# Kernel tuning notes

Hardware: AMD Instinct MI355X
Metric: run time of the kernel (lower is better)

## Reference

```python
import jax, jax.numpy as jnp
import numpy as np

R = 128          # input voxel grid resolution
N = 200000
C_IN = 128
C_OUT = 256
G = 32           # group-norm groups
EPS = 1e-5


def _build_sparse_structure():
    """Generate random sparse voxel coords, downsample map, and 3x3x3 neighbor table."""
    rng = np.random.default_rng(0)
    lin = rng.choice(R ** 3, size=N, replace=False)
    cx, cy, cz = lin // (R * R), (lin // R) % R, lin % R
    # downsample by 2: coords // 2 on a (R//2)^3 grid
    Rd = R // 2
    key = ((cx // 2) * Rd + (cy // 2)) * Rd + (cz // 2)
    uk, inv = np.unique(key, return_inverse=True)   # uk sorted
    M = len(uk)
    dx, dy, dz = uk // (Rd * Rd), (uk // Rd) % Rd, uk % Rd
    # 27-neighbor table for submanifold 3x3x3 conv on the downsampled coords
    nbr = np.full((M, 27), -1, np.int32)
    k = 0
    for ox in (-1, 0, 1):
        for oy in (-1, 0, 1):
            for oz in (-1, 0, 1):
                nx, ny, nz = dx + ox, dy + oy, dz + oz
                valid = (nx >= 0) & (nx < Rd) & (ny >= 0) & (ny < Rd) & (nz >= 0) & (nz < Rd)
                nkey = (nx * Rd + ny) * Rd + nz
                pos = np.clip(np.searchsorted(uk, nkey), 0, M - 1)
                found = valid & (uk[pos] == nkey)
                nbr[:, k] = np.where(found, pos, -1).astype(np.int32)
                k += 1
    return inv.astype(np.int32), nbr, M


def setup_inputs() -> dict:
    pool_seg, nbr_idx, M = _build_sparse_structure()
    key = jax.random.key(0)
    ks = jax.random.split(key, 12)
    f32 = jnp.float32
    feats = jax.random.normal(ks[0], (N, C_IN), f32)
    s1 = float(1.0 / np.sqrt(27 * C_IN))
    s2 = float(1.0 / np.sqrt(27 * C_OUT))
    return {
        "feats": feats,
        "gn1_w": 1.0 + 0.1 * jax.random.normal(ks[1], (C_IN,), f32),
        "gn1_b": 0.1 * jax.random.normal(ks[2], (C_IN,), f32),
        "W1": jax.random.normal(ks[3], (27, C_IN, C_OUT), f32) * s1,
        "b1": 0.01 * jax.random.normal(ks[4], (C_OUT,), f32),
        "gn2_w": 1.0 + 0.1 * jax.random.normal(ks[5], (C_OUT,), f32),
        "gn2_b": 0.1 * jax.random.normal(ks[6], (C_OUT,), f32),
        "W2": jax.random.normal(ks[7], (27, C_OUT, C_OUT), f32) * s2,
        "b2": 0.01 * jax.random.normal(ks[8], (C_OUT,), f32),
        "Wskip": jax.random.normal(ks[9], (C_IN, C_OUT), f32) * float(1.0 / np.sqrt(C_IN)),
        "bskip": 0.01 * jax.random.normal(ks[10], (C_OUT,), f32),
        "pool_seg": jnp.asarray(pool_seg),
        "nbr_idx": jnp.asarray(nbr_idx),
        "num_down": int(M),
    }


def _group_norm(x, gamma, beta):
    # batch size 1: normalize each group over all voxels and its channels
    n, c = x.shape
    xg = x.reshape(n, G, c // G)
    mu = xg.mean(axis=(0, 2), keepdims=True)
    var = xg.var(axis=(0, 2), keepdims=True)
    xn = (xg - mu) * jax.lax.rsqrt(var + EPS)
    return xn.reshape(n, c) * gamma + beta


def _sparse_conv3(x, W, b, nbr_idx):
    # submanifold 3x3x3 conv: out[i] = sum_k W[k] @ x[nbr[i,k]] (missing nbr -> 0)
    idx = jnp.maximum(nbr_idx, 0)
    mask = (nbr_idx >= 0).astype(x.dtype)
    acc = jnp.zeros((x.shape[0], W.shape[2]), x.dtype)
    for k in range(27):
        acc = acc + (x[idx[:, k]] * mask[:, k:k + 1]) @ W[k]
    return acc + b


def reference(feats, gn1_w, gn1_b, W1, b1, gn2_w, gn2_b, W2, b2, Wskip, bskip,
              pool_seg, nbr_idx, num_down):
    # act_layers: GroupNorm32 + SiLU on the full-resolution sparse tensor
    h = jax.nn.silu(_group_norm(feats, gn1_w, gn1_b))
    # SparseDownsample(2): average features of voxels sharing a coord//2 cell
    cnt = jax.ops.segment_sum(jnp.ones((feats.shape[0], 1), feats.dtype),
                              pool_seg, num_segments=num_down)
    inv_cnt = 1.0 / jnp.maximum(cnt, 1.0)
    h_d = jax.ops.segment_sum(h, pool_seg, num_segments=num_down) * inv_cnt
    x_d = jax.ops.segment_sum(feats, pool_seg, num_segments=num_down) * inv_cnt
    # out_layers: conv3 -> GN -> SiLU -> conv3
    h1 = _sparse_conv3(h_d, W1, b1, nbr_idx)
    h2 = jax.nn.silu(_group_norm(h1, gn2_w, gn2_b))
    h3 = _sparse_conv3(h2, W2, b2, nbr_idx)
    # skip: 1x1 sparse conv on downsampled input, then add (same coord set)
    skip = x_d @ Wskip + bskip
    return h3 + skip
```

## Files before the change

### kernel.cpp

```cpp
#include <hip/hip_runtime.h>
#include <hip/hip_bf16.h>
#include <stdint.h>

typedef __hip_bfloat16 bf16;
typedef __attribute__((ext_vector_type(8))) __bf16 bf16x8;
typedef __attribute__((ext_vector_type(4))) float f32x4;

#define GN_EPS 1e-5f

__device__ __forceinline__ float silu_f(float x) {
  return x / (1.f + __expf(-x));
}

__device__ __forceinline__ float ldf(const void* p, size_t i, int f) {
  return f ? ((const float*)p)[i]
           : __bfloat162float(((const bf16*)p)[i]);
}

__device__ __forceinline__ void llds16(const void* g, void* l) {
  __builtin_amdgcn_global_load_lds(
      (const __attribute__((address_space(1))) unsigned int*)g,
      (__attribute__((address_space(3))) unsigned int*)l, 16, 0, 0);
}

__device__ __forceinline__ void gload16(bf16x8& d, const bf16* addr) {
  asm volatile("global_load_dwordx4 %0, %1, off"
               : "=&v"(d) : "v"(addr) : "memory");
}

__global__ void detect_k(const void* __restrict__ gn1w, int* __restrict__ flag) {
  if (threadIdx.x == 0 && blockIdx.x == 0) {
    const unsigned short* u = (const unsigned short*)gn1w;
    float mx = 0.f;
    for (int i = 0; i < 128; ++i) {
      unsigned int b = ((unsigned int)u[i]) << 16;
      float v = __uint_as_float(b);
      v = fabsf(v);
      if (!isnan(v) && v > mx) mx = v;
    }
    flag[0] = (mx > 1e4f) ? 1 : 0;
  }
}

__global__ void transpose_k(const void* __restrict__ in, bf16* __restrict__ out,
                            int CI, int CO, const int* __restrict__ flagp) {
  const int f = *flagp;
  int k = blockIdx.y;
  int ntco = CO >> 5;
  int tci = blockIdx.x / ntco, tco = blockIdx.x % ntco;
  __shared__ float t[32][33];
  int tx = threadIdx.x & 31, ty = threadIdx.x >> 5;
  size_t base = (size_t)k * CI * CO;
  bf16* dst = out + base;
#pragma unroll
  for (int j = 0; j < 4; ++j)
    t[ty + 8 * j][tx] =
        ldf(in, base + (size_t)(tci * 32 + ty + 8 * j) * CO + tco * 32 + tx, f);
  __syncthreads();
#pragma unroll
  for (int j = 0; j < 4; ++j)
    dst[(size_t)tci * (CO * 32) + (size_t)(tco * 32 + ty + 8 * j) * 32 + tx] =
        __float2bfloat16(t[tx][ty + 8 * j]);
}

__global__ void gn_stats_k(const void* __restrict__ x, float* __restrict__ raw,
                           int rows, int C, const int* __restrict__ flagp) {
  const int f = *flagp;
  int tid = threadIdx.x;
  int rpb = 256 / C;
  int c = tid & (C - 1);
  int stripe = tid / C;
  float s = 0.f, sq = 0.f;
  for (int r = blockIdx.x * rpb + stripe; r < rows; r += gridDim.x * rpb) {
    float v = ldf(x, (size_t)r * C + c, f);
    s += v; sq += v * v;
  }
  __shared__ float ls[256], lq[256];
  ls[tid] = s; lq[tid] = sq;
  __syncthreads();
  if (tid < 32) {
    int per = C >> 5;
    float as = 0.f, aq = 0.f;
    for (int st = 0; st < rpb; ++st)
      for (int e = 0; e < per; ++e) {
        int idx = st * C + tid * per + e;
        as += ls[idx]; aq += lq[idx];
      }
    atomicAdd(&raw[tid], as);
    atomicAdd(&raw[32 + tid], aq);
  }
}

__global__ void gn_fin_k(const float* __restrict__ raw, float* __restrict__ fin,
                         float count) {
  int g = threadIdx.x;
  if (g < 32) {
    float mu = raw[g] / count;
    float var = fmaxf(raw[32 + g] / count - mu * mu, 0.f);
    fin[g] = mu;
    fin[32 + g] = rsqrtf(var + GN_EPS);
  }
}

__global__ void slots_k(const int* __restrict__ seg, int* __restrict__ cnt,
                        int* __restrict__ slots, int N) {
  int i = blockIdx.x * 256 + threadIdx.x;
  if (i >= N) return;
  int s = seg[i];
  int p = atomicAdd(&cnt[s], 1);
  if (p < 8) slots[s * 8 + p] = i;
}

__global__ void down_k(const void* __restrict__ feats, const int* __restrict__ slots,
                       const int* __restrict__ cnt, const float* __restrict__ fin1,
                       const void* __restrict__ gw, const void* __restrict__ gb,
                       bf16* __restrict__ xd, bf16* __restrict__ hd, int M,
                       const int* __restrict__ flagp) {
  const int f = *flagp;
  int cell = blockIdx.x * 2 + (threadIdx.x >> 7);
  int c = threadIdx.x & 127;
  if (cell >= M) return;
  int n = min(cnt[cell], 8);
  int g = c >> 2;
  float mu = fin1[g], is = fin1[32 + g];
  float w = ldf(gw, c, f), b = ldf(gb, c, f);
  float xs = 0.f, hs = 0.f;
  for (int j = 0; j < n; ++j) {
    int v = slots[cell * 8 + j];
    float fv = ldf(feats, (size_t)v * 128 + c, f);
    xs += fv;
    hs += silu_f((fv - mu) * is * w + b);
  }
  float inv = 1.f / (float)max(n, 1);
  xd[(size_t)cell * 128 + c] = __float2bfloat16(xs * inv);
  hd[(size_t)cell * 128 + c] = __float2bfloat16(hs * inv);
}

__global__ void act2_k(bf16* __restrict__ h, const float* __restrict__ fin2,
                       const void* __restrict__ gw, const void* __restrict__ gb,
                       size_t total8, const int* __restrict__ flagp) {
  const int f = *flagp;
  size_t i = (size_t)blockIdx.x * 256 + threadIdx.x;
  if (i >= total8) return;
  int c0 = (int)((i * 8) & 255);
  int g = c0 >> 3;
  float mu = fin2[g], is = fin2[32 + g];
  bf16x8 v = *reinterpret_cast<bf16x8*>(h + i * 8);
  bf16x8 o;
#pragma unroll
  for (int j = 0; j < 8; ++j) {
    float x = (float)v[j];
    float t = (x - mu) * is * ldf(gw, c0 + j, f) + ldf(gb, c0 + j, f);
    o[j] = (__bf16)silu_f(t);
  }
  *reinterpret_cast<bf16x8*>(h + i * 8) = o;
}

template <int CIN, bool SKIP>
__global__ __launch_bounds__(512, 2) void conv_k(
    const bf16* __restrict__ A, const bf16* __restrict__ Wt,
    const void* __restrict__ bias, const void* __restrict__ bias2,
    const bf16* __restrict__ Xd, const int* __restrict__ nbr,
    void* __restrict__ out, int M, int nwg, const void* __restrict__ zp,
    const int* __restrict__ biasflagp, const int* __restrict__ outflagp) {
  constexpr int NCB = CIN / 32;
  constexpr int LOG_NCB = (CIN == 256) ? 3 : 2;
  constexpr int NT = 27 * NCB + (SKIP ? 4 : 0);
  __shared__ alignas(16) char smem[24576 + 10368];
  char* Aring = smem;
  int* nbrT = (int*)(smem + 24576);

  const int bflag = *biasflagp, oflag = *outflagp;
  const int tid = threadIdx.x;
  const int wave = tid >> 6, lane = tid & 63;
  const bool wlo = (wave < 6);

  int bid = blockIdx.x;
  int q = nwg >> 3, r8 = nwg & 7, xcd = bid & 7, ix = bid >> 3;
  int wg = (xcd < r8 ? xcd * (q + 1) : r8 * (q + 1) + (xcd - r8) * q) + ix;
  const int row0 = wg * 96;

  for (int i = tid; i < 27 * 96; i += 512) {
    int k = i / 96, r = i - k * 96;
    int g = row0 + r;
    int v = -1;
    if (g < M) v = nbr[(size_t)g * 27 + k];
    nbrT[i] = v;
  }
  __syncthreads();

  const int srow = lane >> 2;
  const int schk = lane & 3;

  auto stageA = [&](int t) {
    if (!wlo) return;
    char* Asl = Aring + (size_t)(t & 3) * 6144;
    const bool isW = (!SKIP) || (t < 27 * NCB);
    const int kk = t >> LOG_NCB;
    const int cb = isW ? (t & (NCB - 1)) : (t - 27 * NCB);
    const int cink = isW ? CIN : 128;
    const bf16* Ab = isW ? A : Xd;
    const int koff = cb * 32;
    int r = wave * 16 + srow;
    int src;
    if (isW) src = nbrT[kk * 96 + r];
    else { int g = row0 + r; src = (g < M) ? g : -1; }
    int lc = schk ^ ((r >> 1) & 3);
    const bf16* ga = (src >= 0) ? Ab + (size_t)src * cink + koff + lc * 8
                                : (const bf16*)zp;
    llds16(ga, Asl + (size_t)wave * 1024);
  };

  const int mrow = lane & 15, quad = lane >> 4;
  const int wr = wave >> 2, wc = wave & 3;
  const int cswz = (quad ^ ((mrow >> 1) & 3)) * 16;

  int beoff[4];
#pragma unroll
  for (int j = 0; j < 4; ++j)
    beoff[j] = (wc * 64 + j * 16 + mrow) * 32 + quad * 8;

  auto loadB = [&](bf16x8 (&dst)[4], int t) {
    const bool isW = (!SKIP) || (t < 27 * NCB);
    const int kk = t >> LOG_NCB;
    const int cb = isW ? (t & (NCB - 1)) : (t - 27 * NCB);
    const bf16* base = Wt +
        (isW ? (size_t)kk * (256 * CIN) : (size_t)27 * (256 * CIN)) +
        (size_t)cb * (256 * 32);
#pragma unroll
    for (int j = 0; j < 4; ++j) gload16(dst[j], base + beoff[j]);
  };

  f32x4 acc[3][4] = {};

  auto compute = [&](int t, const bf16x8 (&bv)[4]) {
    const char* As = Aring + (size_t)(t & 3) * 6144 +
                     (size_t)(wr * 48 + mrow) * 64 + cswz;
    bf16x8 af[3];
#pragma unroll
    for (int i = 0; i < 3; ++i)
      af[i] = *reinterpret_cast<const bf16x8*>(As + i * (16 * 64));
    __builtin_amdgcn_s_setprio(1);
#pragma unroll
    for (int i = 0; i < 3; ++i)
#pragma unroll
      for (int j = 0; j < 4; ++j)
        acc[i][j] = __builtin_amdgcn_mfma_f32_16x16x32_bf16(af[i], bv[j],
                                                            acc[i][j], 0, 0, 0);
    __builtin_amdgcn_s_setprio(0);
  };

#define VMW(a, b)                                                        \
  do {                                                                   \
    if (wlo) asm volatile("s_waitcnt vmcnt(" #a ")" ::: "memory");       \
    else     asm volatile("s_waitcnt vmcnt(" #b ")" ::: "memory");       \
    __builtin_amdgcn_sched_barrier(0);                                   \
  } while (0)
#define BAR() __builtin_amdgcn_s_barrier()

  bf16x8 bX[4], bY[4];

  stageA(0); stageA(1);
  loadB(bX, 0);

#pragma unroll 1
  for (int u = 0; u < NT / 2 - 1; ++u) {
    const int s = 2 * u;
    loadB(bY, s + 1);
    stageA(s + 2);
    VMW(5, 4);
    BAR();
    compute(s, bX);
    loadB(bX, s + 2);
    stageA(s + 3);
    VMW(6, 4);
    BAR();
    compute(s + 1, bY);
  }
  loadB(bY, NT - 1);
  VMW(4, 4);
  BAR();
  compute(NT - 2, bX);
  VMW(0, 0);
  BAR();
  compute(NT - 1, bY);

#undef VMW
#undef BAR

#pragma unroll
  for (int j = 0; j < 4; ++j) {
    int col = wc * 64 + j * 16 + mrow;
    float bvl = ldf(bias, col, bflag);
    if (SKIP) bvl += ldf(bias2, col, bflag);
#pragma unroll
    for (int i = 0; i < 3; ++i) {
      int rb = row0 + wr * 48 + i * 16 + quad * 4;
#pragma unroll
      for (int r = 0; r < 4; ++r) {
        int row = rb + r;
        if (row < M) {
          size_t idx = (size_t)row * 256 + col;
          float val = acc[i][j][r] + bvl;
          if (oflag) ((float*)out)[idx] = val;
          else ((bf16*)out)[idx] = __float2bfloat16(val);
        }
      }
    }
  }
}

extern "C" void kernel_launch(void* const* d_in, const int* in_sizes, int n_in,
                              void* d_out, int out_size, void* d_ws, size_t ws_size,
                              hipStream_t stream) {
  const void* feats = d_in[0];
  const void* gn1w = d_in[1];
  const void* gn1b = d_in[2];
  const void* W1 = d_in[3];
  const void* b1 = d_in[4];
  const void* gn2w = d_in[5];
  const void* gn2b = d_in[6];
  const void* W2 = d_in[7];
  const void* b2 = d_in[8];
  const void* Wsk = d_in[9];
  const void* bsk = d_in[10];
  const int* pool = (const int*)d_in[11];
  const int* nbr = (const int*)d_in[12];
  const int N = in_sizes[0] / 128;
  const int M = out_size / 256;

  char* ws = (char*)d_ws;
  auto aup = [](size_t x) { return (x + 255) & ~(size_t)255; };
  float* raw1 = (float*)(ws + 0);
  float* raw2 = (float*)(ws + 256);
  int* flag = (int*)(ws + 512);
  int* zeroflag = (int*)(ws + 516);
  const void* zp = (const void*)(ws + 768);
  int* cnt = (int*)(ws + 1024);
  size_t o = aup(1024 + (size_t)M * 4);
  float* fin1 = (float*)(ws + o); o += 256;
  float* fin2 = (float*)(ws + o); o += 256;
  int* slots = (int*)(ws + o); o = aup(o + (size_t)M * 32);
  bf16* xd = (bf16*)(ws + o); o += (size_t)M * 256;
  bf16* hd = (bf16*)(ws + o); o += (size_t)M * 256;
  bf16* h1 = (bf16*)(ws + o); o += (size_t)M * 512;
  bf16* wt1 = (bf16*)(ws + o); o += (size_t)27 * 256 * 128 * 2;
  bf16* wt2 = (bf16*)(ws + o); o += ((size_t)27 * 256 * 256 + 256 * 128) * 2;
  (void)ws_size; (void)n_in;

  hipMemsetAsync(ws, 0, 1024 + (size_t)M * 4, stream);

  detect_k<<<1, 64, 0, stream>>>(gn1w, flag);

  transpose_k<<<dim3(4 * 8, 27), 256, 0, stream>>>(W1, wt1, 128, 256, flag);
  transpose_k<<<dim3(8 * 8, 27), 256, 0, stream>>>(W2, wt2, 256, 256, flag);
  transpose_k<<<dim3(4 * 8, 1), 256, 0, stream>>>(
      Wsk, wt2 + (size_t)27 * 256 * 256, 128, 256, flag);

  gn_stats_k<<<512, 256, 0, stream>>>(feats, raw1, N, 128, flag);
  gn_fin_k<<<1, 64, 0, stream>>>(raw1, fin1, (float)N * 4.f);

  slots_k<<<(N + 255) / 256, 256, 0, stream>>>(pool, cnt, slots, N);
  down_k<<<(M + 1) / 2, 256, 0, stream>>>(feats, slots, cnt, fin1, gn1w, gn1b,
                                          xd, hd, M, flag);

  const int nwg = (M + 95) / 96;

  conv_k<128, false><<<nwg, 512, 0, stream>>>(
      hd, wt1, b1, nullptr, nullptr, nbr, h1, M, nwg, zp, flag, zeroflag);

  gn_stats_k<<<512, 256, 0, stream>>>(h1, raw2, M, 256, zeroflag);
  gn_fin_k<<<1, 64, 0, stream>>>(raw2, fin2, (float)M * 8.f);
  act2_k<<<(int)(((size_t)M * 32 + 255) / 256), 256, 0, stream>>>(
      h1, fin2, gn2w, gn2b, (size_t)M * 32, flag);

  conv_k<256, true><<<nwg, 512, 0, stream>>>(
      h1, wt2, b2, bsk, xd, nbr, d_out, M, nwg, zp, flag, flag);
}
```

Before: 1.652 ms.

## Enlarge conv tile to 192 rows and 64-wide K steps with double buffer

The sparse conv kernel now processes 192 output rows per workgroup instead of 96, and 64 input channels per pipeline step instead of 32. All 8 waves now stage A rows with a new XOR swizzle, in place of only six waves before, and the A ring shrinks from four slots to two, which requires extra barriers after each compute. Larger tiles double weight reuse per B fragment and halve the number of pipeline steps. The cost is far more accumulator registers (24 f32x4 per thread), much larger LDS use, fewer workgroups, and more synchronisation that may limit overlap and occupancy.

New measurement: 1.555 ms. -5.9%, faster.

```diff
diff --git a/kernel.cpp b/kernel.cpp
--- a/kernel.cpp
+++ b/kernel.cpp
@@ -163,125 +163,135 @@
     const bf16* __restrict__ Xd, const int* __restrict__ nbr,
     void* __restrict__ out, int M, int nwg, const void* __restrict__ zp,
     const int* __restrict__ biasflagp, const int* __restrict__ outflagp) {
-  constexpr int NCB = CIN / 32;
-  constexpr int LOG_NCB = (CIN == 256) ? 3 : 2;
-  constexpr int NT = 27 * NCB + (SKIP ? 4 : 0);
-  __shared__ alignas(16) char smem[24576 + 10368];
+  constexpr int NCB = CIN / 64;
+  constexpr int LOG_NCB = (CIN == 256) ? 2 : 1;
+  constexpr int NT = 27 * NCB + (SKIP ? 2 : 0);
+  __shared__ alignas(16) char smem[49152 + 20736];
   char* Aring = smem;
-  int* nbrT = (int*)(smem + 24576);
+  int* nbrT = (int*)(smem + 49152);
 
   const int bflag = *biasflagp, oflag = *outflagp;
   const int tid = threadIdx.x;
   const int wave = tid >> 6, lane = tid & 63;
-  const bool wlo = (wave < 6);
 
   int bid = blockIdx.x;
   int q = nwg >> 3, r8 = nwg & 7, xcd = bid & 7, ix = bid >> 3;
   int wg = (xcd < r8 ? xcd * (q + 1) : r8 * (q + 1) + (xcd - r8) * q) + ix;
-  const int row0 = wg * 96;
-
-  for (int i = tid; i < 27 * 96; i += 512) {
-    int k = i / 96, r = i - k * 96;
+  const int row0 = wg * 192;
+
+  for (int i = tid; i < 27 * 192; i += 512) {
+    int r = i / 27, k = i - r * 27;
     int g = row0 + r;
-    int v = -1;
-    if (g < M) v = nbr[(size_t)g * 27 + k];
-    nbrT[i] = v;
+    int v = (g < M) ? nbr[(size_t)row0 * 27 + i] : -1;
+    nbrT[k * 192 + r] = v;
   }
   __syncthreads();
 
-  const int srow = lane >> 2;
-  const int schk = lane & 3;
+  const int prow = lane >> 3;
+  const int schk = lane & 7;
+  const int gc = schk ^ prow;
 
   auto stageA = [&](int t) {
-    if (!wlo) return;
-    char* Asl = Aring + (size_t)(t & 3) * 6144;
+    char* Asl = Aring + (size_t)(t & 1) * 24576;
     const bool isW = (!SKIP) || (t < 27 * NCB);
     const int kk = t >> LOG_NCB;
     const int cb = isW ? (t & (NCB - 1)) : (t - 27 * NCB);
     const int cink = isW ? CIN : 128;
     const bf16* Ab = isW ? A : Xd;
-    const int koff = cb * 32;
-    int r = wave * 16 + srow;
-    int src;
-    if (isW) src = nbrT[kk * 96 + r];
-    else { int g = row0 + r; src = (g < M) ? g : -1; }
-    int lc = schk ^ ((r >> 1) & 3);
-    const bf16* ga = (src >= 0) ? Ab + (size_t)src * cink + koff + lc * 8
-                                : (const bf16*)zp;
-    llds16(ga, Asl + (size_t)wave * 1024);
+    const int koff = cb * 64;
+#pragma unroll
+    for (int p = 0; p < 3; ++p) {
+      int panel = wave * 3 + p;
+      int r = panel * 8 + prow;
+      int src;
+      if (isW) src = nbrT[kk * 192 + r];
+      else { int g = row0 + r; src = (g < M) ? g : -1; }
+      const bf16* ga = (src >= 0) ? Ab + (size_t)src * cink + koff + gc * 8
+                                  : (const bf16*)zp;
+      llds16(ga, Asl + (size_t)panel * 1024);
+    }
   };
 
   const int mrow = lane & 15, quad = lane >> 4;
   const int wr = wave >> 2, wc = wave & 3;
-  const int cswz = (quad ^ ((mrow >> 1) & 3)) * 16;
+  const int sw0 = ((quad) ^ (mrow & 7)) * 16;
+  const int sw1 = ((4 + quad) ^ (mrow & 7)) * 16;
 
   int beoff[4];
 #pragma unroll
   for (int j = 0; j < 4; ++j)
     beoff[j] = (wc * 64 + j * 16 + mrow) * 32 + quad * 8;
 
-  auto loadB = [&](bf16x8 (&dst)[4], int t) {
+  auto loadB = [&](bf16x8 (&dst)[8], int t) {
     const bool isW = (!SKIP) || (t < 27 * NCB);
     const int kk = t >> LOG_NCB;
     const int cb = isW ? (t & (NCB - 1)) : (t - 27 * NCB);
     const bf16* base = Wt +
         (isW ? (size_t)kk * (256 * CIN) : (size_t)27 * (256 * CIN)) +
-        (size_t)cb * (256 * 32);
-#pragma unroll
-    for (int j = 0; j < 4; ++j) gload16(dst[j], base + beoff[j]);
+        (size_t)cb * (256 * 64);
+#pragma unroll
+    for (int ks = 0; ks < 2; ++ks)
+#pragma unroll
+      for (int j = 0; j < 4; ++j)
+        gload16(dst[ks * 4 + j], base + ks * 8192 + beoff[j]);
   };
 
-  f32x4 acc[3][4] = {};
-
-  auto compute = [&](int t, const bf16x8 (&bv)[4]) {
-    const char* As = Aring + (size_t)(t & 3) * 6144 +
-                     (size_t)(wr * 48 + mrow) * 64 + cswz;
-    bf16x8 af[3];
-#pragma unroll
-    for (int i = 0; i < 3; ++i)
-      af[i] = *reinterpret_cast<const bf16x8*>(As + i * (16 * 64));
+  f32x4 acc[6][4] = {};
+
+  auto compute = [&](int t, const bf16x8 (&bv)[8]) {
+    const char* As = Aring + (size_t)(t & 1) * 24576 +
+                     (size_t)(wr * 96 + mrow) * 128;
     __builtin_amdgcn_s_setprio(1);
 #pragma unroll
-    for (int i = 0; i < 3; ++i)
-#pragma unroll
-      for (int j = 0; j < 4; ++j)
-        acc[i][j] = __builtin_amdgcn_mfma_f32_16x16x32_bf16(af[i], bv[j],
+    for (int i = 0; i < 6; ++i) {
+      bf16x8 a0 = *reinterpret_cast<const bf16x8*>(As + i * (16 * 128) + sw0);
+      bf16x8 a1 = *reinterpret_cast<const bf16x8*>(As + i * (16 * 128) + sw1);
+#pragma unroll
+      for (int j = 0; j < 4; ++j) {
+        acc[i][j] = __builtin_amdgcn_mfma_f32_16x16x32_bf16(a0, bv[j],
                                                             acc[i][j], 0, 0, 0);
+        acc[i][j] = __builtin_amdgcn_mfma_f32_16x16x32_bf16(a1, bv[4 + j],
+                                                            acc[i][j], 0, 0, 0);
+      }
+    }
     __builtin_amdgcn_s_setprio(0);
   };
 
-#define VMW(a, b)                                                        \
+#define VMW(n)                                                           \
   do {                                                                   \
-    if (wlo) asm volatile("s_waitcnt vmcnt(" #a ")" ::: "memory");       \
-    else     asm volatile("s_waitcnt vmcnt(" #b ")" ::: "memory");       \
+    asm volatile("s_waitcnt vmcnt(" #n ")" ::: "memory");                \
     __builtin_amdgcn_sched_barrier(0);                                   \
   } while (0)
 #define BAR() __builtin_amdgcn_s_barrier()
 
-  bf16x8 bX[4], bY[4];
-
-  stageA(0); stageA(1);
+  bf16x8 bX[8], bY[8];
+
+  stageA(0);
   loadB(bX, 0);
 
 #pragma unroll 1
   for (int u = 0; u < NT / 2 - 1; ++u) {
     const int s = 2 * u;
     loadB(bY, s + 1);
-    stageA(s + 2);
-    VMW(5, 4);
+    stageA(s + 1);
+    VMW(11);
     BAR();
     compute(s, bX);
+    BAR();
     loadB(bX, s + 2);
-    stageA(s + 3);
-    VMW(6, 4);
+    stageA(s + 2);
+    VMW(11);
     BAR();
     compute(s + 1, bY);
+    BAR();
   }
   loadB(bY, NT - 1);
-  VMW(4, 4);
+  stageA(NT - 1);
+  VMW(11);
   BAR();
   compute(NT - 2, bX);
-  VMW(0, 0);
+  BAR();
+  VMW(0);
   BAR();
   compute(NT - 1, bY);
 
@@ -294,8 +304,8 @@
     float bvl = ldf(bias, col, bflag);
     if (SKIP) bvl += ldf(bias2, col, bflag);
 #pragma unroll
-    for (int i = 0; i < 3; ++i) {
-      int rb = row0 + wr * 48 + i * 16 + quad * 4;
+    for (int i = 0; i < 6; ++i) {
+      int rb = row0 + wr * 96 + i * 16 + quad * 4;
 #pragma unroll
       for (int r = 0; r < 4; ++r) {
         int row = rb + r;
@@ -364,7 +374,7 @@
   down_k<<<(M + 1) / 2, 256, 0, stream>>>(feats, slots, cnt, fin1, gn1w, gn1b,
                                           xd, hd, M, flag);
 
-  const int nwg = (M + 95) / 96;
+  const int nwg = (M + 191) / 192;
 
   conv_k<128, false><<<nwg, 512, 0, stream>>>(
       hd, wt1, b1, nullptr, nullptr, nbr, h1, M, nwg, zp, flag, zeroflag);
```
